# Optimization experiments

Measured on AMD Instinct MI355X. Metric: run time of the kernel, lower is better.

## Reference

```python
import jax, jax.numpy as jnp
import numpy as np
import math

D = 2048  # hidden_size
B, S = 4, 2048
EPS = 1e-5


def _ln(z, g, b):
    m = jnp.mean(z, axis=-1, keepdims=True)
    v = jnp.mean(jnp.square(z - m), axis=-1, keepdims=True)
    return (z - m) * jax.lax.rsqrt(v + EPS) * g + b


def _rotate_half(x):
    h = x.shape[-1] // 2
    return jnp.concatenate([-x[..., h:], x[..., :h]], axis=-1)


def _mas_normalize(logits):
    m = jnp.max(jnp.abs(logits), axis=-1, keepdims=True)
    return logits / (m + 1e-9)


def setup_inputs() -> dict:
    key = jax.random.key(0)
    ks = jax.random.split(key, 12)
    std = 0.02
    return {
        "x": jax.random.normal(ks[0], (B, S, D), dtype=jnp.float32),
        "position_ids": jnp.arange(S, dtype=jnp.int32),
        "ln1_g": jnp.ones((D,), jnp.float32),
        "ln1_b": jnp.zeros((D,), jnp.float32),
        # stacked params for [q, k, v, o]
        "mu_w": std * jax.random.normal(ks[1], (4, D, D), dtype=jnp.float32),
        "mu_b": jnp.zeros((4, D), jnp.float32),
        "proto_w": std * jax.random.normal(ks[2], (4, D, D), dtype=jnp.float32),
        "gate": jnp.zeros((4, D), jnp.float32),
        "pt_w": std * jax.random.normal(ks[3], (4, D, D), dtype=jnp.float32),
        "pln_g": jnp.ones((4, D), jnp.float32),
        "pln_b": jnp.zeros((4, D), jnp.float32),
        "incoming": std * jax.random.normal(ks[4], (4, D, D), dtype=jnp.float32),
    }


def reference(x, position_ids, ln1_g, ln1_b, mu_w, mu_b, proto_w, gate,
              pt_w, pln_g, pln_b, incoming):
    d = x.shape[-1]
    inv_sqrt_d = 1.0 / math.sqrt(d)

    # proto_state = proto_weight + LN(Linear(incoming))  per module [4, D, D]
    prc = jnp.einsum('nij,noj->nio', incoming, pt_w)
    proto_state = proto_w + _ln(prc, pln_g[:, None, :], pln_b[:, None, :])

    ln1_out = _ln(x, ln1_g, ln1_b)            # [B,S,D]
    ctx = jnp.mean(ln1_out, axis=1)           # [B,D]

    # qkv computation outputs: silu(ln1_out @ mu_w.T + mu_b) for n in {q,k,v}
    comp = jax.nn.silu(jnp.einsum('bsd,nod->nbso', ln1_out, mu_w[:3])
                       + mu_b[:3][:, None, None, :])            # [3,B,S,D]
    # routing from context vector
    match_ctx = jnp.einsum('bd,nod->nbo', ctx, proto_state[:3]) * inv_sqrt_d
    routing = match_ctx + gate[:3][:, None, :]                  # [3,B,D]
    gating = _mas_normalize(routing)
    masked = gating[:, :, None, :] * comp                       # [3,B,S,D]
    q, k, v = masked[0], masked[1], masked[2]

    # RoPE over full hidden dim (num_heads == 1)
    seq = position_ids.shape[0]
    inv_freq = 1.0 / (10000.0 ** (jnp.arange(0, d, 2, dtype=jnp.float32) / d))
    t = jnp.arange(seq, dtype=jnp.float32)
    freqs = t[:, None] * inv_freq[None, :]
    emb = jnp.concatenate([freqs, freqs], axis=-1)              # [S,D]
    cos = jnp.cos(emb)[position_ids]
    sin = jnp.sin(emb)[position_ids]
    q = q * cos + _rotate_half(q) * sin
    k = k * cos + _rotate_half(k) * sin

    # causal single-head attention, scale 1/sqrt(head_dim=D)
    scores = jnp.einsum('bqd,bkd->bqk', q, k) * inv_sqrt_d      # [B,S,S]
    causal = jnp.tril(jnp.ones((seq, seq), dtype=bool))
    scores = jnp.where(causal, scores, jnp.finfo(scores.dtype).min)
    probs = jax.nn.softmax(scores, axis=-1)
    attn_out = jnp.einsum('bqk,bkd->bqd', probs, v)             # [B,S,D]

    # output SPL + routing
    ctx_o = jnp.mean(attn_out, axis=1)
    c_o = jax.nn.silu(jnp.einsum('bsd,od->bso', attn_out, mu_w[3]) + mu_b[3])
    match_o = jnp.einsum('bd,od->bo', ctx_o, proto_state[3]) * inv_sqrt_d
    gating_o = _mas_normalize(match_o + gate[3])
    x_out = x + gating_o[:, None, :] * c_o
    return x_out
```

## Files before the change

### kernel.cpp

```cpp
#include <hip/hip_runtime.h>
#include <hip/hip_bf16.h>

#define Dh 2048
#define Bh 4
#define Sh 2048
#define NROW 8192
#define HALF 1024
#define INV_SQRT_D 0.022097086912079608f
#define LNEPS 1e-5f

typedef __hip_bfloat16 bf16;
typedef short short8 __attribute__((ext_vector_type(8)));
typedef float f32x4 __attribute__((ext_vector_type(4)));

__device__ inline float warp_sum(float x) {
#pragma unroll
  for (int o = 32; o > 0; o >>= 1) x += __shfl_down(x, o);
  return x;
}
__device__ inline float warp_max(float x) {
#pragma unroll
  for (int o = 32; o > 0; o >>= 1) x = fmaxf(x, __shfl_down(x, o));
  return x;
}
__device__ inline float block_sum(float x, float* sm4) {
  x = warp_sum(x);
  int w = threadIdx.x >> 6;
  if ((threadIdx.x & 63) == 0) sm4[w] = x;
  __syncthreads();
  float r = sm4[0] + sm4[1] + sm4[2] + sm4[3];
  __syncthreads();
  return r;
}
__device__ inline float block_max(float x, float* sm4) {
  x = warp_max(x);
  int w = threadIdx.x >> 6;
  if ((threadIdx.x & 63) == 0) sm4[w] = x;
  __syncthreads();
  float r = fmaxf(fmaxf(sm4[0], sm4[1]), fmaxf(sm4[2], sm4[3]));
  __syncthreads();
  return r;
}

__device__ inline void gload_lds16(const void* g, void* lds) {
  __builtin_amdgcn_global_load_lds(
      (const __attribute__((address_space(1))) unsigned int*)(unsigned long long)g,
      (__attribute__((address_space(3))) unsigned int*)(unsigned long long)lds,
      16, 0, 0);
}

template <int MODE>
__global__ __launch_bounds__(512) void pgemm(
    const bf16* __restrict__ Aall, const bf16* __restrict__ Ball,
    void* __restrict__ Call, int N, int K, int lda, int ldb,
    long sAz, long sBz, long sCz,
    const float* __restrict__ e0, const float* __restrict__ e1,
    const float* __restrict__ e2) {
  const int gx = gridDim.x, gy = gridDim.y;
  const int nwg = gx * gy * gridDim.z;
  const int fid = blockIdx.x + gx * (blockIdx.y + gy * blockIdx.z);
  const int cpx = nwg >> 3;
  const int wk = (fid & 7) * cpx + (fid >> 3);
  const int mx = wk % gx;
  const int rest = wk / gx;
  const int my = rest % gy;
  const int bm0 = mx * 256;
  const int bn0 = my * 256;
  if (MODE == 2 && bn0 > bm0 + 255) return;
  const int z = rest / gy;
  const bf16* A = Aall + (long)z * sAz;
  const bf16* B = Ball + (long)z * sBz;

  __shared__ __align__(16) char smem[98304];
  const int tid = threadIdx.x;
  const int l = tid & 63, w = tid >> 6;
  const int wr = w >> 2, wc = w & 3;

  f32x4 acc[8][4] = {};

  const int nt = (MODE == 3) ? ((bm0 + 256) >> 5) : (K >> 5);

  const int sg = (((l & 3) ^ ((l >> 3) & 3)) << 3);

  auto stageA = [&](int tt, int half) {
    char* dst = smem + (tt % 3) * 16384 + (half << 13) + (w << 10);
    int row = (half << 7) + (w << 4) + (l >> 2);
    gload_lds16(A + (long)(bm0 + row) * lda + (tt << 5) + sg, dst);
  };
  auto stageB = [&](int tt, int half) {
    char* dst = smem + 49152 + (tt % 3) * 16384 + (half << 13) + (w << 10);
    int row = (half << 7) + (w << 4) + (l >> 2);
    gload_lds16(B + (long)(bn0 + row) * ldb + (tt << 5) + sg, dst);
  };

  stageA(0, 0); stageA(0, 1); stageB(0, 0); stageB(0, 1);
  if (nt > 1) { stageA(1, 0); stageA(1, 1); stageB(1, 0); stageB(1, 1); }
  if (nt > 1) asm volatile("s_waitcnt vmcnt(4)" ::: "memory");
  else        asm volatile("s_waitcnt vmcnt(0)" ::: "memory");
  __builtin_amdgcn_sched_barrier(0);
  asm volatile("s_barrier" ::: "memory");

#define PH(FR0, FR1, STG)                                                     \
  do {                                                                        \
    short8 xa0 = *(const short8*)(Ab + abyte + FR0 * 1024);                   \
    short8 xa1 = *(const short8*)(Ab + abyte + FR1 * 1024);                   \
    STG;                                                                      \
    __builtin_amdgcn_s_setprio(1);                                            \
    acc[FR0][0] = __builtin_amdgcn_mfma_f32_16x16x32_bf16(xa0, bfv0, acc[FR0][0], 0, 0, 0); \
    acc[FR1][0] = __builtin_amdgcn_mfma_f32_16x16x32_bf16(xa1, bfv0, acc[FR1][0], 0, 0, 0); \
    acc[FR0][1] = __builtin_amdgcn_mfma_f32_16x16x32_bf16(xa0, bfv1, acc[FR0][1], 0, 0, 0); \
    acc[FR1][1] = __builtin_amdgcn_mfma_f32_16x16x32_bf16(xa1, bfv1, acc[FR1][1], 0, 0, 0); \
    acc[FR0][2] = __builtin_amdgcn_mfma_f32_16x16x32_bf16(xa0, bfv2, acc[FR0][2], 0, 0, 0); \
    acc[FR1][2] = __builtin_amdgcn_mfma_f32_16x16x32_bf16(xa1, bfv2, acc[FR1][2], 0, 0, 0); \
    acc[FR0][3] = __builtin_amdgcn_mfma_f32_16x16x32_bf16(xa0, bfv3, acc[FR0][3], 0, 0, 0); \
    acc[FR1][3] = __builtin_amdgcn_mfma_f32_16x16x32_bf16(xa1, bfv3, acc[FR1][3], 0, 0, 0); \
    __builtin_amdgcn_s_setprio(0);                                            \
  } while (0)

  const int rslot = (((l >> 4) ^ ((l >> 1) & 3)) << 4);

  for (int t = 0; t < nt; ++t) {
    const char* Ab = smem + (t % 3) * 16384;
    const char* Bb = smem + 49152 + (t % 3) * 16384;
    const int abyte = (((wr << 7) + (l & 15)) << 6) + rslot;
    const int bbyte = (((wc << 6) + (l & 15)) << 6) + rslot;

    short8 bfv0 = *(const short8*)(Bb + bbyte + 0 * 1024);
    short8 bfv1 = *(const short8*)(Bb + bbyte + 1 * 1024);
    short8 bfv2 = *(const short8*)(Bb + bbyte + 2 * 1024);
    short8 bfv3 = *(const short8*)(Bb + bbyte + 3 * 1024);

    PH(0, 1, if (t + 2 < nt) { stageA(t + 2, 0); stageB(t + 2, 0); });
    PH(2, 3, if (t + 2 < nt) { stageA(t + 2, 1); stageB(t + 2, 1); });
    PH(4, 5, );
    PH(6, 7, );
    if (t < nt - 1) {
      if (t + 2 < nt) asm volatile("s_waitcnt vmcnt(4)" ::: "memory");
      else            asm volatile("s_waitcnt vmcnt(0)" ::: "memory");
      __builtin_amdgcn_sched_barrier(0);
      asm volatile("s_barrier" ::: "memory");
    }
  }
#undef PH

  const int lc = l & 15, lr4 = (l >> 4) << 2;
#pragma unroll
  for (int fr = 0; fr < 8; ++fr) {
    int gr0 = bm0 + (wr << 7) + fr * 16 + lr4;
#pragma unroll
    for (int fc = 0; fc < 4; ++fc) {
      int gc = bn0 + (wc << 6) + fc * 16 + lc;
#pragma unroll
      for (int qv = 0; qv < 4; ++qv) {
        int gr = gr0 + qv;
        float a = acc[fr][fc][qv];
        if (MODE == 0) {
          ((float*)Call + (long)z * sCz)[(long)gr * N + gc] = a;
        } else if (MODE == 1) {
          float val = a + e0[z * Dh + gc];
          float sil = val / (1.f + __expf(-val));
          int bb = gr >> 11;
          float g = e1[(z * Bh + bb) * Dh + gc];
          ((bf16*)Call + (long)z * sCz)[(long)gr * N + gc] =
              __float2bfloat16(sil * g);
        } else if (MODE == 2) {
          ((float*)Call + (long)z * sCz)[(long)gr * N + gc] = a * INV_SQRT_D;
        } else if (MODE == 3) {
          ((bf16*)Call + (long)z * sCz)[(long)gr * N + gc] = __float2bfloat16(a);
        } else {
          float val = a + e0[gc];
          float sil = val / (1.f + __expf(-val));
          int bb = gr >> 11;
          ((float*)Call)[(long)gr * N + gc] =
              e2[(long)gr * N + gc] + e1[bb * Dh + gc] * sil;
        }
      }
    }
  }
}

__global__ __launch_bounds__(256) void cvt3_kernel(
    const float* __restrict__ s0, const float* __restrict__ s1,
    const float* __restrict__ s2, bf16* __restrict__ o0, bf16* __restrict__ o1,
    bf16* __restrict__ o2, long n) {
  const float* in = (blockIdx.y == 0) ? s0 : (blockIdx.y == 1) ? s1 : s2;
  bf16* out = (blockIdx.y == 0) ? o0 : (blockIdx.y == 1) ? o1 : o2;
  long i = ((long)blockIdx.x * 256 + threadIdx.x) * 4;
  if (i >= n) return;
  float4 v = *(const float4*)(in + i);
  out[i + 0] = __float2bfloat16(v.x);
  out[i + 1] = __float2bfloat16(v.y);
  out[i + 2] = __float2bfloat16(v.z);
  out[i + 3] = __float2bfloat16(v.w);
}

__global__ __launch_bounds__(256) void transpose_kernel(const bf16* __restrict__ in,
                                                        bf16* __restrict__ out) {
  __shared__ bf16 t[64][65];
  int b = blockIdx.z;
  int s0 = blockIdx.x * 64, d0 = blockIdx.y * 64;
  const bf16* ib = in + (long)b * Sh * Dh;
  bf16* ob = out + (long)b * Sh * Dh;
  int tx = threadIdx.x & 63, ty = threadIdx.x >> 6;
#pragma unroll
  for (int r = ty; r < 64; r += 4) t[r][tx] = ib[(long)(s0 + r) * Dh + d0 + tx];
  __syncthreads();
#pragma unroll
  for (int r = ty; r < 64; r += 4) ob[(long)(d0 + r) * Sh + s0 + tx] = t[tx][r];
}

__global__ __launch_bounds__(256) void ln1_kernel(const float* __restrict__ x,
    const float* __restrict__ g, const float* __restrict__ b, bf16* __restrict__ out) {
  __shared__ float sm4[4];
  long r = blockIdx.x;
  const float* row = x + r * Dh;
  float v[8];
  float s = 0.f, s2 = 0.f;
#pragma unroll
  for (int c = 0; c < 8; ++c) {
    float t = row[threadIdx.x + c * 256];
    v[c] = t; s += t; s2 += t * t;
  }
  s = block_sum(s, sm4);
  s2 = block_sum(s2, sm4);
  float mean = s * (1.f / Dh);
  float rstd = rsqrtf(s2 * (1.f / Dh) - mean * mean + LNEPS);
#pragma unroll
  for (int c = 0; c < 8; ++c) {
    int o = threadIdx.x + c * 256;
    out[r * Dh + o] = __float2bfloat16((v[c] - mean) * rstd * g[o] + b[o]);
  }
}

__global__ __launch_bounds__(256) void meanrow_kernel(const bf16* __restrict__ in,
                                                      float* __restrict__ outbd) {
  int gid = blockIdx.x * 256 + threadIdx.x;
  int s0 = blockIdx.y * 128;
  long base = ((long)(gid >> 11) * Sh + s0) * Dh + (gid & 2047);
  float s = 0.f;
  for (int t = 0; t < 128; ++t) s += __bfloat162float(in[base + (long)t * Dh]);
  atomicAdd(&outbd[gid], s * (1.f / Sh));
}

__global__ __launch_bounds__(256) void route_kernel(
    const float* __restrict__ prc, const float* __restrict__ proto_w,
    const float* __restrict__ pln_g, const float* __restrict__ pln_b,
    const float* __restrict__ gate, const float* __restrict__ ctx,
    float* __restrict__ routing, float* __restrict__ ps3) {
  __shared__ float sm4[4];
  int i = blockIdx.x, n = blockIdx.y;
  long rb = ((long)n * Dh + i) * Dh;
  float v[8];
  float s = 0.f, s2 = 0.f;
#pragma unroll
  for (int c = 0; c < 8; ++c) {
    float t = prc[rb + threadIdx.x + c * 256];
    v[c] = t; s += t; s2 += t * t;
  }
  s = block_sum(s, sm4);
  s2 = block_sum(s2, sm4);
  float mean = s * (1.f / Dh);
  float rstd = rsqrtf(s2 * (1.f / Dh) - mean * mean + LNEPS);
  if (n == 3) {
#pragma unroll
    for (int c = 0; c < 8; ++c) {
      int o = threadIdx.x + c * 256;
      float ps = proto_w[rb + o] + (v[c] - mean) * rstd * pln_g[3 * Dh + o] + pln_b[3 * Dh + o];
      ps3[(long)i * Dh + o] = ps;
    }
  } else {
    float acc[4] = {0.f, 0.f, 0.f, 0.f};
#pragma unroll
    for (int c = 0; c < 8; ++c) {
      int o = threadIdx.x + c * 256;
      float ps = proto_w[rb + o] + (v[c] - mean) * rstd * pln_g[n * Dh + o] + pln_b[n * Dh + o];
#pragma unroll
      for (int b = 0; b < 4; ++b) acc[b] += ps * ctx[b * Dh + o];
    }
    for (int b = 0; b < 4; ++b) {
      float r = block_sum(acc[b], sm4);
      if (threadIdx.x == 0)
        routing[(n * 4 + b) * Dh + i] = r * INV_SQRT_D + gate[n * Dh + i];
    }
  }
}

__global__ __launch_bounds__(256) void route_o_kernel(
    const float* __restrict__ ps3, const float* __restrict__ ctxo,
    const float* __restrict__ gate, float* __restrict__ routing) {
  __shared__ float sm4[4];
  int i = blockIdx.x;
  float acc[4] = {0.f, 0.f, 0.f, 0.f};
#pragma unroll
  for (int c = 0; c < 8; ++c) {
    int o = threadIdx.x + c * 256;
    float p = ps3[(long)i * Dh + o];
#pragma unroll
    for (int b = 0; b < 4; ++b) acc[b] += p * ctxo[b * Dh + o];
  }
  for (int b = 0; b < 4; ++b) {
    float r = block_sum(acc[b], sm4);
    if (threadIdx.x == 0)
      routing[(12 + b) * Dh + i] = r * INV_SQRT_D + gate[3 * Dh + i];
  }
}

__global__ __launch_bounds__(256) void masnorm_kernel(const float* __restrict__ rin,
                                                      float* __restrict__ gout) {
  __shared__ float sm4[4];
  long r = blockIdx.x;
  float m = 0.f;
#pragma unroll
  for (int c = 0; c < 8; ++c)
    m = fmaxf(m, fabsf(rin[r * Dh + threadIdx.x + c * 256]));
  m = block_max(m, sm4);
  float inv = 1.f / (m + 1e-9f);
#pragma unroll
  for (int c = 0; c < 8; ++c) {
    int o = threadIdx.x + c * 256;
    gout[r * Dh + o] = rin[r * Dh + o] * inv;
  }
}

__global__ __launch_bounds__(256) void rope_table_kernel(float* __restrict__ cosT,
                                                         float* __restrict__ sinT) {
  int idx = blockIdx.x * 256 + threadIdx.x;
  int t = idx >> 10, f = idx & 1023;
  float inv_freq = expf(-(float)f * (9.210340371976184f / 1024.f));
  float ang = (float)t * inv_freq;
  cosT[idx] = cosf(ang);
  sinT[idx] = sinf(ang);
}

__global__ __launch_bounds__(256) void rope_kernel(bf16* __restrict__ q, bf16* __restrict__ k,
    const int* __restrict__ pos, const float* __restrict__ cosT,
    const float* __restrict__ sinT) {
  long r = blockIdx.x;
  int s = (int)(r & (Sh - 1));
  int p = pos[s];
#pragma unroll
  for (int c = 0; c < 4; ++c) {
    int t = threadIdx.x + c * 256;
    float cv = cosT[(long)p * HALF + t];
    float sv = sinT[(long)p * HALF + t];
    long i1 = r * Dh + t, i2 = i1 + HALF;
    float q1 = __bfloat162float(q[i1]), q2 = __bfloat162float(q[i2]);
    q[i1] = __float2bfloat16(q1 * cv - q2 * sv);
    q[i2] = __float2bfloat16(q2 * cv + q1 * sv);
    float k1 = __bfloat162float(k[i1]), k2 = __bfloat162float(k[i2]);
    k[i1] = __float2bfloat16(k1 * cv - k2 * sv);
    k[i2] = __float2bfloat16(k2 * cv + k1 * sv);
  }
}

__global__ __launch_bounds__(256) void softmax_kernel(const float* __restrict__ scores,
                                                      bf16* __restrict__ probs) {
  __shared__ float buf[Sh];
  __shared__ float sm4[4];
  long r = blockIdx.x;
  int qi = (int)(r & (Sh - 1));
  const float* row = scores + r * (long)Sh;
  bf16* prow = probs + r * (long)Sh;
  int n = qi + 1;
  float m = -3.0e38f;
  for (int o = threadIdx.x; o < n; o += 256) {
    float x = row[o]; buf[o] = x; m = fmaxf(m, x);
  }
  m = block_max(m, sm4);
  float s = 0.f;
  for (int o = threadIdx.x; o < n; o += 256) {
    float e = __expf(buf[o] - m); buf[o] = e; s += e;
  }
  s = block_sum(s, sm4);
  float inv = 1.f / s;
  for (int o = threadIdx.x; o < n; o += 256) prow[o] = __float2bfloat16(buf[o] * inv);
  for (int o = n + (int)threadIdx.x; o < Sh; o += 256) prow[o] = __float2bfloat16(0.f);
}

extern "C" void kernel_launch(void* const* d_in, const int* in_sizes, int n_in,
                              void* d_out, int out_size, void* d_ws, size_t ws_size,
                              hipStream_t stream) {
  const float* x       = (const float*)d_in[0];
  const int*   pos     = (const int*)d_in[1];
  const float* ln1_g   = (const float*)d_in[2];
  const float* ln1_b   = (const float*)d_in[3];
  const float* mu_w    = (const float*)d_in[4];
  const float* mu_b    = (const float*)d_in[5];
  const float* proto_w = (const float*)d_in[6];
  const float* gate    = (const float*)d_in[7];
  const float* pt_w    = (const float*)d_in[8];
  const float* pln_g   = (const float*)d_in[9];
  const float* pln_b   = (const float*)d_in[10];
  const float* incoming= (const float*)d_in[11];

  char* w = (char*)d_ws;
  const long BF = 33554432L;
  bf16*  ln1    = (bf16*)(w);
  bf16*  qb     = (bf16*)(w + BF);
  bf16*  kb     = (bf16*)(w + 2 * BF);
  bf16*  vb     = (bf16*)(w + 3 * BF);
  bf16*  attn   = (bf16*)(w + 4 * BF);
  bf16*  mu_wb  = (bf16*)(w + 5 * BF);
  bf16*  ptw_b  = (bf16*)(w + 6 * BF);
  bf16*  vT     = ptw_b;
  bf16*  inc_b  = (bf16*)(w + 7 * BF);
  bf16*  probs  = inc_b;
  float* ps3    = (float*)(w + 8 * BF);
  float* cosT   = (float*)(w + 8 * BF + 16777216L);
  float* sinT   = cosT + (long)Sh * HALF;
  float* ctx    = sinT + (long)Sh * HALF;
  float* ctxo   = ctx + Bh * Dh;
  float* routing= ctxo + Bh * Dh;
  float* gating = routing + 16 * Dh;
  float* scores = (float*)d_out;

  const long DD4 = 4L * Dh * Dh;

  hipMemsetAsync(ctx, 0, 2L * Bh * Dh * sizeof(float), stream);

  rope_table_kernel<<<(Sh * HALF) / 256, 256, 0, stream>>>(cosT, sinT);
  cvt3_kernel<<<dim3(DD4 / 1024, 3), 256, 0, stream>>>(
      mu_w, incoming, pt_w, mu_wb, inc_b, ptw_b, DD4);
  ln1_kernel<<<NROW, 256, 0, stream>>>(x, ln1_g, ln1_b, ln1);
  meanrow_kernel<<<dim3(32, 16), 256, 0, stream>>>(ln1, ctx);
  pgemm<0><<<dim3(8, 8, 4), 512, 0, stream>>>(
      inc_b, ptw_b, scores, Dh, Dh, Dh, Dh,
      (long)Dh * Dh, (long)Dh * Dh, (long)Dh * Dh, nullptr, nullptr, nullptr);
  route_kernel<<<dim3(Dh, 4), 256, 0, stream>>>(scores, proto_w, pln_g, pln_b,
                                                gate, ctx, routing, ps3);
  masnorm_kernel<<<12, 256, 0, stream>>>(routing, gating);
  pgemm<1><<<dim3(32, 8, 3), 512, 0, stream>>>(
      ln1, mu_wb, qb, Dh, Dh, Dh, Dh,
      0L, (long)Dh * Dh, (long)NROW * Dh, mu_b, gating, nullptr);
  rope_kernel<<<NROW, 256, 0, stream>>>(qb, kb, pos, cosT, sinT);
  pgemm<2><<<dim3(8, 8, 4), 512, 0, stream>>>(
      qb, kb, scores, Sh, Dh, Dh, Dh,
      (long)Sh * Dh, (long)Sh * Dh, (long)Sh * Sh, nullptr, nullptr, nullptr);
  softmax_kernel<<<Bh * Sh, 256, 0, stream>>>(scores, probs);
  transpose_kernel<<<dim3(32, 32, 4), 256, 0, stream>>>(vb, vT);
  pgemm<3><<<dim3(8, 8, 4), 512, 0, stream>>>(
      probs, vT, attn, Dh, Sh, Sh, Sh,
      (long)Sh * Sh, (long)Dh * Sh, (long)Sh * Dh, nullptr, nullptr, nullptr);
  meanrow_kernel<<<dim3(32, 16), 256, 0, stream>>>(attn, ctxo);
  route_o_kernel<<<Dh, 256, 0, stream>>>(ps3, ctxo, gate, routing);
  masnorm_kernel<<<4, 256, 0, stream>>>(routing + 12 * Dh, gating + 12 * Dh);
  pgemm<4><<<dim3(32, 8, 1), 512, 0, stream>>>(
      attn, mu_wb + 3L * Dh * Dh, d_out, Dh, Dh, Dh, Dh,
      0L, 0L, 0L, mu_b + 3 * Dh, gating + 12 * Dh, x);
}
```

Before: 710.8 us.

## Restructure GEMM main loop into two barrier-synchronized phases; drop XCD tile remap

Splits each K-step into two halves. Each half loads four A fragments from LDS, issues half of the next tile's global-to-LDS copies, then uses explicit s_barrier and lgkmcnt waits before a block of 16 MFMAs at raised priority. This replaces the interleaved PH macro schedule. It also removes the remapping that spread consecutive workgroups across the 8 XCDs, going back to plain blockIdx tile assignment, which can hurt L2 locality. The extra barriers add synchronization cost in exchange for keeping the waves in lockstep.

```diff
diff --git a/kernel.cpp b/kernel.cpp
--- a/kernel.cpp
+++ b/kernel.cpp
@@ -56,18 +56,10 @@
     long sAz, long sBz, long sCz,
     const float* __restrict__ e0, const float* __restrict__ e1,
     const float* __restrict__ e2) {
-  const int gx = gridDim.x, gy = gridDim.y;
-  const int nwg = gx * gy * gridDim.z;
-  const int fid = blockIdx.x + gx * (blockIdx.y + gy * blockIdx.z);
-  const int cpx = nwg >> 3;
-  const int wk = (fid & 7) * cpx + (fid >> 3);
-  const int mx = wk % gx;
-  const int rest = wk / gx;
-  const int my = rest % gy;
-  const int bm0 = mx * 256;
-  const int bn0 = my * 256;
+  const int bm0 = blockIdx.x * 256;
+  const int bn0 = blockIdx.y * 256;
   if (MODE == 2 && bn0 > bm0 + 255) return;
-  const int z = rest / gy;
+  const int z = blockIdx.z;
   const bf16* A = Aall + (long)z * sAz;
   const bf16* B = Ball + (long)z * sBz;
 
@@ -100,24 +92,13 @@
   __builtin_amdgcn_sched_barrier(0);
   asm volatile("s_barrier" ::: "memory");
 
-#define PH(FR0, FR1, STG)                                                     \
-  do {                                                                        \
-    short8 xa0 = *(const short8*)(Ab + abyte + FR0 * 1024);                   \
-    short8 xa1 = *(const short8*)(Ab + abyte + FR1 * 1024);                   \
-    STG;                                                                      \
-    __builtin_amdgcn_s_setprio(1);                                            \
-    acc[FR0][0] = __builtin_amdgcn_mfma_f32_16x16x32_bf16(xa0, bfv0, acc[FR0][0], 0, 0, 0); \
-    acc[FR1][0] = __builtin_amdgcn_mfma_f32_16x16x32_bf16(xa1, bfv0, acc[FR1][0], 0, 0, 0); \
-    acc[FR0][1] = __builtin_amdgcn_mfma_f32_16x16x32_bf16(xa0, bfv1, acc[FR0][1], 0, 0, 0); \
-    acc[FR1][1] = __builtin_amdgcn_mfma_f32_16x16x32_bf16(xa1, bfv1, acc[FR1][1], 0, 0, 0); \
-    acc[FR0][2] = __builtin_amdgcn_mfma_f32_16x16x32_bf16(xa0, bfv2, acc[FR0][2], 0, 0, 0); \
-    acc[FR1][2] = __builtin_amdgcn_mfma_f32_16x16x32_bf16(xa1, bfv2, acc[FR1][2], 0, 0, 0); \
-    acc[FR0][3] = __builtin_amdgcn_mfma_f32_16x16x32_bf16(xa0, bfv3, acc[FR0][3], 0, 0, 0); \
-    acc[FR1][3] = __builtin_amdgcn_mfma_f32_16x16x32_bf16(xa1, bfv3, acc[FR1][3], 0, 0, 0); \
-    __builtin_amdgcn_s_setprio(0);                                            \
-  } while (0)
-
   const int rslot = (((l >> 4) ^ ((l >> 1) & 3)) << 4);
+
+#define MFMA4(FR)                                                             \
+  acc[FR][0] = __builtin_amdgcn_mfma_f32_16x16x32_bf16(xa##FR, bfv0, acc[FR][0], 0, 0, 0); \
+  acc[FR][1] = __builtin_amdgcn_mfma_f32_16x16x32_bf16(xa##FR, bfv1, acc[FR][1], 0, 0, 0); \
+  acc[FR][2] = __builtin_amdgcn_mfma_f32_16x16x32_bf16(xa##FR, bfv2, acc[FR][2], 0, 0, 0); \
+  acc[FR][3] = __builtin_amdgcn_mfma_f32_16x16x32_bf16(xa##FR, bfv3, acc[FR][3], 0, 0, 0);
 
   for (int t = 0; t < nt; ++t) {
     const char* Ab = smem + (t % 3) * 16384;
@@ -129,11 +110,30 @@
     short8 bfv1 = *(const short8*)(Bb + bbyte + 1 * 1024);
     short8 bfv2 = *(const short8*)(Bb + bbyte + 2 * 1024);
     short8 bfv3 = *(const short8*)(Bb + bbyte + 3 * 1024);
-
-    PH(0, 1, if (t + 2 < nt) { stageA(t + 2, 0); stageB(t + 2, 0); });
-    PH(2, 3, if (t + 2 < nt) { stageA(t + 2, 1); stageB(t + 2, 1); });
-    PH(4, 5, );
-    PH(6, 7, );
+    short8 xa0 = *(const short8*)(Ab + abyte + 0 * 1024);
+    short8 xa1 = *(const short8*)(Ab + abyte + 1 * 1024);
+    short8 xa2 = *(const short8*)(Ab + abyte + 2 * 1024);
+    short8 xa3 = *(const short8*)(Ab + abyte + 3 * 1024);
+    if (t + 2 < nt) { stageA(t + 2, 0); stageB(t + 2, 0); }
+    asm volatile("s_barrier" ::: "memory");
+    asm volatile("s_waitcnt lgkmcnt(0)" ::: "memory");
+    __builtin_amdgcn_sched_barrier(0);
+    __builtin_amdgcn_s_setprio(1);
+    MFMA4(0) MFMA4(1) MFMA4(2) MFMA4(3)
+    __builtin_amdgcn_s_setprio(0);
+    asm volatile("s_barrier" ::: "memory");
+
+    short8 xa4 = *(const short8*)(Ab + abyte + 4 * 1024);
+    short8 xa5 = *(const short8*)(Ab + abyte + 5 * 1024);
+    short8 xa6 = *(const short8*)(Ab + abyte + 6 * 1024);
+    short8 xa7 = *(const short8*)(Ab + abyte + 7 * 1024);
+    if (t + 2 < nt) { stageA(t + 2, 1); stageB(t + 2, 1); }
+    asm volatile("s_barrier" ::: "memory");
+    asm volatile("s_waitcnt lgkmcnt(0)" ::: "memory");
+    __builtin_amdgcn_sched_barrier(0);
+    __builtin_amdgcn_s_setprio(1);
+    MFMA4(4) MFMA4(5) MFMA4(6) MFMA4(7)
+    __builtin_amdgcn_s_setprio(0);
     if (t < nt - 1) {
       if (t + 2 < nt) asm volatile("s_waitcnt vmcnt(4)" ::: "memory");
       else            asm volatile("s_waitcnt vmcnt(0)" ::: "memory");
@@ -141,7 +141,7 @@
       asm volatile("s_barrier" ::: "memory");
     }
   }
-#undef PH
+#undef MFMA4
 
   const int lc = l & 15, lr4 = (l >> 4) << 2;
 #pragma unroll
```

After: 721.3 us. No clear change (+1.5%).
